# Optimization experiments

Hardware: AMD Instinct MI355X
Metric: run time of the kernel (lower is better)

Reference implementation:

```python
import jax, jax.numpy as jnp
import numpy as np

K = 5  # kernel_size

def _extract_patches(x):
    # TF extract_patches, SAME padding, stride 1, rate 1.
    # x: (B,H,W,C) -> (B,H,W,K*K,C); patch index i is row-major over (kh,kw),
    # channel d is the fastest-varying dim, matching TF's flatten order.
    p = K // 2
    xp = jnp.pad(x, ((0, 0), (p, p), (p, p), (0, 0)))
    B, H, W, C = x.shape
    pats = [xp[:, i:i + H, j:j + W, :] for i in range(K) for j in range(K)]
    return jnp.stack(pats, axis=3)

def setup_inputs() -> dict:
    key = jax.random.key(0)
    k1, k2, k3, k4 = jax.random.split(key, 4)
    B, H, W, C, F = 8, 250, 250, 4, 16
    return {
        "x": jax.random.normal(k1, (B, H, W, C), jnp.float32),
        "kernel": jax.random.normal(k2, (K, K, C, F), jnp.float32) * 0.05,
        "quad_kernel": jax.random.normal(k3, (C, K * K, K * K, F), jnp.float32) * 0.02,
        "bias": jax.random.normal(k4, (F,), jnp.float32) * 0.01,
    }

def reference(x, kernel, quad_kernel, bias):
    # Quadratic (Volterra) term: V[b,h,w,o] = sum_{i,j,d} p[bhwid] p[bhwjd] W[d,i,j,o]
    # (einsum 'abcid,abcjd,dijo->abcdo' followed by reduce_sum over d).
    patches = _extract_patches(x)  # (B,H,W,25,C)
    C = x.shape[-1]
    quad = 0.0
    for d in range(C):  # small fixed channel loop avoids a (B,H,W,25,C,F) intermediate
        pd = patches[..., d]                                   # (B,H,W,25)
        s = jnp.einsum('bhwj,ijo->bhwio', pd, quad_kernel[d])  # (B,H,W,25,F)
        quad = quad + jnp.einsum('bhwi,bhwio->bhwo', pd, s)    # (B,H,W,F)
    # Linear conv term (SAME padding, stride 1)
    lin = jax.lax.conv_general_dilated(
        x, kernel, window_strides=(1, 1), padding='SAME',
        dimension_numbers=('NHWC', 'HWIO', 'NHWC'))
    return quad + lin + bias
```

## Files before the change

### kernel.cpp

```cpp
#include <hip/hip_runtime.h>
#include <utility>


typedef _Float16 half2 __attribute__((ext_vector_type(2)));
typedef _Float16 half4 __attribute__((ext_vector_type(4)));
typedef _Float16 half8 __attribute__((ext_vector_type(8)));
typedef float floatx4 __attribute__((ext_vector_type(4)));

#define BB 8
#define HH 250
#define WW 250
#define NF 16
#define NSLOT_PAIR 181
#define NSLOT_LIN  13
#define NCHUNK     49
#define NFRAG      (NCHUNK * 64)

#define TW 64
#define TH 8
#define XW (TW + 4)
#define XH (TH + 4)
#define XSZ (XW * XH)

__host__ __device__ constexpr int slot_i(int s) {
    int i = 0, base = 0;
    while (base + (13 - (i >> 1)) <= s) { base += 13 - (i >> 1); ++i; }
    return i;
}
__host__ __device__ constexpr int slot_g(int s) {
    int i = 0, base = 0;
    while (base + (13 - (i >> 1)) <= s) { base += 13 - (i >> 1); ++i; }
    return (i >> 1) + (s - base);
}

__global__ void prep_frags(const float* __restrict__ lin_w,
                           const float* __restrict__ quad_w,
                           _Float16* __restrict__ fragB) {
    const int c = blockIdx.x;
    const int lane = threadIdx.x;
    const int n = lane & 15;
    const int d = lane >> 4;
    half8 frag;
    #pragma unroll
    for (int e = 0; e < 8; ++e) {
        const int f = c * 8 + e;
        const int s = f >> 1, hf = f & 1;
        float v = 0.f;
        if (s < NSLOT_PAIR) {
            int i = 0, base = 0;
            while (base + (13 - (i >> 1)) <= s) { base += 13 - (i >> 1); ++i; }
            const int g = (i >> 1) + (s - base);
            const int j = 2 * g + hf;
            if (j == i)
                v = quad_w[((d * 25 + i) * 25 + i) * 16 + n];
            else if (j > i && j < 25)
                v = quad_w[((d * 25 + i) * 25 + j) * 16 + n]
                  + quad_w[((d * 25 + j) * 25 + i) * 16 + n];
        } else if (s < NSLOT_PAIR + NSLOT_LIN) {
            const int j = 2 * (s - NSLOT_PAIR) + hf;
            if (j < 25) v = lin_w[(j * 4 + d) * 16 + n];
        }
        frag[e] = (_Float16)v;
    }
    *(half8*)(fragB + (c * 64 + lane) * 8) = frag;
}

__device__ __forceinline__ half2 pk(float lo, float hi) {
    return __builtin_bit_cast(half2, __builtin_amdgcn_cvt_pkrtz(lo, hi));
}

template<int S>
__device__ __forceinline__ half2 slotval(const half2 (&pd2)[13]) {
    if constexpr (S < NSLOT_PAIR) {
        constexpr int i = slot_i(S), g = slot_g(S);
        constexpr int ir = i >> 1, ih = i & 1;
        const half2 src = pd2[ir];
        const half2 bi = {src[ih], src[ih]};
        return bi * pd2[g];
    } else if constexpr (S < NSLOT_PAIR + NSLOT_LIN) {
        return pd2[S - NSLOT_PAIR];
    } else {
        return half2{(_Float16)0.f, (_Float16)0.f};
    }
}

template<int C>
__device__ __forceinline__ half8 make_frag(const half2 (&pd2)[13]) {
    const half2 a0 = slotval<C * 4 + 0>(pd2);
    const half2 a1 = slotval<C * 4 + 1>(pd2);
    const half2 a2 = slotval<C * 4 + 2>(pd2);
    const half2 a3 = slotval<C * 4 + 3>(pd2);
    const half4 lo = __builtin_shufflevector(a0, a1, 0, 1, 2, 3);
    const half4 hi = __builtin_shufflevector(a2, a3, 0, 1, 2, 3);
    return __builtin_shufflevector(lo, hi, 0, 1, 2, 3, 4, 5, 6, 7);
}

template<size_t... Cs>
__device__ __forceinline__ void gemm_all(
    const half2 (&p0)[13], const half2 (&p1)[13],
    const half2 (&p2)[13], const half2 (&p3)[13],
    const _Float16* sBlane,
    floatx4& a0, floatx4& a1, floatx4& a2, floatx4& a3,
    std::index_sequence<Cs...>) {
    (([&] {
        constexpr int C = (int)Cs;
        const half8 bf = *(const half8*)(sBlane + C * 64 * 8);
        a0 = __builtin_amdgcn_mfma_f32_16x16x32_f16(make_frag<C>(p0), bf, a0, 0, 0, 0);
        a1 = __builtin_amdgcn_mfma_f32_16x16x32_f16(make_frag<C>(p1), bf, a1, 0, 0, 0);
        a2 = __builtin_amdgcn_mfma_f32_16x16x32_f16(make_frag<C>(p2), bf, a2, 0, 0, 0);
        a3 = __builtin_amdgcn_mfma_f32_16x16x32_f16(make_frag<C>(p3), bf, a3, 0, 0, 0);
    }()), ...);
}

__device__ __forceinline__ void patch_from_lds(const float* xt, int base,
                                               half2 (&pd2)[13]) {
    float pf[26];
    pf[25] = 0.f;
    #pragma unroll
    for (int kh = 0; kh < 5; ++kh)
        #pragma unroll
        for (int kw = 0; kw < 5; ++kw)
            pf[kh * 5 + kw] = xt[base + kh * XW + kw];
    #pragma unroll
    for (int t = 0; t < 13; ++t) pd2[t] = pk(pf[2 * t], pf[2 * t + 1]);
}

__global__ __launch_bounds__(512, 4) void convquad_gemm(
    const float* __restrict__ x,
    const float* __restrict__ bias,
    const _Float16* __restrict__ fragB,
    float* __restrict__ out)
{
    __shared__ float xt[4 * XSZ];
    __shared__ __align__(16) _Float16 sB[NFRAG * 8];

    const int w0 = blockIdx.x * TW;
    const int h0 = blockIdx.y * TH;
    const int b  = blockIdx.z;

    {
        const float4* src = (const float4*)fragB;
        float4* dst = (float4*)sB;
        #pragma unroll
        for (int t = threadIdx.x; t < NFRAG * 8 / 8; t += 512) dst[t] = src[t];
    }

    #pragma unroll 2
    for (int p = threadIdx.x; p < XSZ; p += 512) {
        const int hh = p / XW, ww = p % XW;
        const int r = h0 + hh - 2, c = w0 + ww - 2;
        float4 v = make_float4(0.f, 0.f, 0.f, 0.f);
        if ((unsigned)r < (unsigned)HH && (unsigned)c < (unsigned)WW)
            v = ((const float4*)x)[(b * HH + r) * WW + c];
        xt[0 * XSZ + p] = v.x;
        xt[1 * XSZ + p] = v.y;
        xt[2 * XSZ + p] = v.z;
        xt[3 * XSZ + p] = v.w;
    }
    __syncthreads();

    const int lane = threadIdx.x & 63;
    const int wave = threadIdx.x >> 6;
    const int m = lane & 15;
    const int q = lane >> 4;

    const int base0 = q * XSZ + wave * XW + m;
    half2 pd0[13], pd1[13], pd2[13], pd3[13];
    patch_from_lds(xt, base0,      pd0);
    patch_from_lds(xt, base0 + 16, pd1);
    patch_from_lds(xt, base0 + 32, pd2);
    patch_from_lds(xt, base0 + 48, pd3);

    const float bo = bias[m];
    floatx4 acc0 = {bo, bo, bo, bo};
    floatx4 acc1 = acc0, acc2 = acc0, acc3 = acc0;

    gemm_all(pd0, pd1, pd2, pd3, sB + lane * 8,
             acc0, acc1, acc2, acc3, std::make_index_sequence<NCHUNK>{});

    const int h = h0 + wave;
    if (h < HH) {
        const int rowbase = (b * HH + h) * WW;
        #pragma unroll
        for (int r = 0; r < 4; ++r) {
            const int wA = w0 + q * 4 + r;
            if (wA < WW) out[(rowbase + wA) * NF + m] = acc0[r];
            const int wB = w0 + 16 + q * 4 + r;
            if (wB < WW) out[(rowbase + wB) * NF + m] = acc1[r];
            const int wC = w0 + 32 + q * 4 + r;
            if (wC < WW) out[(rowbase + wC) * NF + m] = acc2[r];
            const int wD = w0 + 48 + q * 4 + r;
            if (wD < WW) out[(rowbase + wD) * NF + m] = acc3[r];
        }
    }
}

extern "C" void kernel_launch(void* const* d_in, const int* in_sizes, int n_in,
                              void* d_out, int out_size, void* d_ws, size_t ws_size,
                              hipStream_t stream) {
    const float* x      = (const float*)d_in[0];
    const float* lin_w  = (const float*)d_in[1];
    const float* quad_w = (const float*)d_in[2];
    const float* bias   = (const float*)d_in[3];
    float* out = (float*)d_out;
    _Float16* fragB = (_Float16*)d_ws;

    prep_frags<<<dim3(NCHUNK), dim3(64), 0, stream>>>(lin_w, quad_w, fragB);

    dim3 grid((WW + TW - 1) / TW, (HH + TH - 1) / TH, BB);
    convquad_gemm<<<grid, dim3(512), 0, stream>>>(x, bias, fragB, out);
}
```

Baseline: 104.0 us.

## Make GEMM kernel persistent with register-prefetched next tile input

Replaces the one-block-per-tile grid with 512 persistent blocks that each process two tiles. The weight fragments are loaded into LDS only once per block, and the next tile's input halo is prefetched into registers while the current tile's MFMA work runs. The goal is to cut the repeated sB fill and hide global load latency, at the cost of extra barriers and higher register pressure.

```diff
diff --git a/kernel.cpp b/kernel.cpp
--- a/kernel.cpp
+++ b/kernel.cpp
@@ -21,6 +21,12 @@
 #define XW (TW + 4)
 #define XH (TH + 4)
 #define XSZ (XW * XH)
+
+#define NBLK     512
+#define NTILE_W  4
+#define NTILE_H  32
+#define NTILES   (BB * NTILE_H * NTILE_W)
+#define NT       (NTILES / NBLK)
 
 __host__ __device__ constexpr int slot_i(int s) {
     int i = 0, base = 0;
@@ -125,6 +131,49 @@
     for (int t = 0; t < 13; ++t) pd2[t] = pk(pf[2 * t], pf[2 * t + 1]);
 }
 
+__device__ __forceinline__ void tile_coords(int T, int& b, int& h0, int& w0) {
+    b = T >> 7;
+    const int rem = T & 127;
+    h0 = (rem >> 2) * TH;
+    w0 = (rem & 3) * TW;
+}
+
+__device__ __forceinline__ void xload_regs(const float* __restrict__ x,
+                                           int b, int h0, int w0,
+                                           float4& v0, float4& v1) {
+    const int p0 = threadIdx.x;
+    {
+        const int hh = p0 / XW, ww = p0 % XW;
+        const int r = h0 + hh - 2, c = w0 + ww - 2;
+        v0 = make_float4(0.f, 0.f, 0.f, 0.f);
+        if ((unsigned)r < (unsigned)HH && (unsigned)c < (unsigned)WW)
+            v0 = ((const float4*)x)[(b * HH + r) * WW + c];
+    }
+    const int p1 = p0 + 512;
+    v1 = make_float4(0.f, 0.f, 0.f, 0.f);
+    if (p1 < XSZ) {
+        const int hh = p1 / XW, ww = p1 % XW;
+        const int r = h0 + hh - 2, c = w0 + ww - 2;
+        if ((unsigned)r < (unsigned)HH && (unsigned)c < (unsigned)WW)
+            v1 = ((const float4*)x)[(b * HH + r) * WW + c];
+    }
+}
+
+__device__ __forceinline__ void xwrite_lds(float* xt, const float4& v0, const float4& v1) {
+    const int p0 = threadIdx.x;
+    xt[0 * XSZ + p0] = v0.x;
+    xt[1 * XSZ + p0] = v0.y;
+    xt[2 * XSZ + p0] = v0.z;
+    xt[3 * XSZ + p0] = v0.w;
+    const int p1 = p0 + 512;
+    if (p1 < XSZ) {
+        xt[0 * XSZ + p1] = v1.x;
+        xt[1 * XSZ + p1] = v1.y;
+        xt[2 * XSZ + p1] = v1.z;
+        xt[3 * XSZ + p1] = v1.w;
+    }
+}
+
 __global__ __launch_bounds__(512, 4) void convquad_gemm(
     const float* __restrict__ x,
     const float* __restrict__ bias,
@@ -134,9 +183,16 @@
     __shared__ float xt[4 * XSZ];
     __shared__ __align__(16) _Float16 sB[NFRAG * 8];
 
-    const int w0 = blockIdx.x * TW;
-    const int h0 = blockIdx.y * TH;
-    const int b  = blockIdx.z;
+    const int lane = threadIdx.x & 63;
+    const int wave = threadIdx.x >> 6;
+    const int m = lane & 15;
+    const int q = lane >> 4;
+    const float bo = bias[m];
+
+    int b, h0, w0;
+    tile_coords(blockIdx.x, b, h0, w0);
+    float4 v0, v1;
+    xload_regs(x, b, h0, w0, v0, v1);
 
     {
         const float4* src = (const float4*)fragB;
@@ -144,53 +200,50 @@
         #pragma unroll
         for (int t = threadIdx.x; t < NFRAG * 8 / 8; t += 512) dst[t] = src[t];
     }
-
-    #pragma unroll 2
-    for (int p = threadIdx.x; p < XSZ; p += 512) {
-        const int hh = p / XW, ww = p % XW;
-        const int r = h0 + hh - 2, c = w0 + ww - 2;
-        float4 v = make_float4(0.f, 0.f, 0.f, 0.f);
-        if ((unsigned)r < (unsigned)HH && (unsigned)c < (unsigned)WW)
-            v = ((const float4*)x)[(b * HH + r) * WW + c];
-        xt[0 * XSZ + p] = v.x;
-        xt[1 * XSZ + p] = v.y;
-        xt[2 * XSZ + p] = v.z;
-        xt[3 * XSZ + p] = v.w;
-    }
+    xwrite_lds(xt, v0, v1);
     __syncthreads();
 
-    const int lane = threadIdx.x & 63;
-    const int wave = threadIdx.x >> 6;
-    const int m = lane & 15;
-    const int q = lane >> 4;
-
-    const int base0 = q * XSZ + wave * XW + m;
-    half2 pd0[13], pd1[13], pd2[13], pd3[13];
-    patch_from_lds(xt, base0,      pd0);
-    patch_from_lds(xt, base0 + 16, pd1);
-    patch_from_lds(xt, base0 + 32, pd2);
-    patch_from_lds(xt, base0 + 48, pd3);
-
-    const float bo = bias[m];
-    floatx4 acc0 = {bo, bo, bo, bo};
-    floatx4 acc1 = acc0, acc2 = acc0, acc3 = acc0;
-
-    gemm_all(pd0, pd1, pd2, pd3, sB + lane * 8,
-             acc0, acc1, acc2, acc3, std::make_index_sequence<NCHUNK>{});
-
-    const int h = h0 + wave;
-    if (h < HH) {
-        const int rowbase = (b * HH + h) * WW;
-        #pragma unroll
-        for (int r = 0; r < 4; ++r) {
-            const int wA = w0 + q * 4 + r;
-            if (wA < WW) out[(rowbase + wA) * NF + m] = acc0[r];
-            const int wB = w0 + 16 + q * 4 + r;
-            if (wB < WW) out[(rowbase + wB) * NF + m] = acc1[r];
-            const int wC = w0 + 32 + q * 4 + r;
-            if (wC < WW) out[(rowbase + wC) * NF + m] = acc2[r];
-            const int wD = w0 + 48 + q * 4 + r;
-            if (wD < WW) out[(rowbase + wD) * NF + m] = acc3[r];
+    #pragma unroll 1
+    for (int t = 0; t < NT; ++t) {
+        int bn, h0n, w0n;
+        if (t + 1 < NT) {
+            tile_coords(blockIdx.x + (t + 1) * NBLK, bn, h0n, w0n);
+            xload_regs(x, bn, h0n, w0n, v0, v1);
+        }
+
+        const int base0 = q * XSZ + wave * XW + m;
+        half2 pd0[13], pd1[13], pd2[13], pd3[13];
+        patch_from_lds(xt, base0,      pd0);
+        patch_from_lds(xt, base0 + 16, pd1);
+        patch_from_lds(xt, base0 + 32, pd2);
+        patch_from_lds(xt, base0 + 48, pd3);
+
+        floatx4 acc0 = {bo, bo, bo, bo};
+        floatx4 acc1 = acc0, acc2 = acc0, acc3 = acc0;
+        gemm_all(pd0, pd1, pd2, pd3, sB + lane * 8,
+                 acc0, acc1, acc2, acc3, std::make_index_sequence<NCHUNK>{});
+
+        const int h = h0 + wave;
+        if (h < HH) {
+            const int rowbase = (b * HH + h) * WW;
+            #pragma unroll
+            for (int r = 0; r < 4; ++r) {
+                const int wA = w0 + q * 4 + r;
+                if (wA < WW) out[(rowbase + wA) * NF + m] = acc0[r];
+                const int wB = w0 + 16 + q * 4 + r;
+                if (wB < WW) out[(rowbase + wB) * NF + m] = acc1[r];
+                const int wC = w0 + 32 + q * 4 + r;
+                if (wC < WW) out[(rowbase + wC) * NF + m] = acc2[r];
+                const int wD = w0 + 48 + q * 4 + r;
+                if (wD < WW) out[(rowbase + wD) * NF + m] = acc3[r];
+            }
+        }
+
+        if (t + 1 < NT) {
+            b = bn; h0 = h0n; w0 = w0n;
+            __syncthreads();
+            xwrite_lds(xt, v0, v1);
+            __syncthreads();
         }
     }
 }
@@ -207,6 +260,5 @@
 
     prep_frags<<<dim3(NCHUNK), dim3(64), 0, stream>>>(lin_w, quad_w, fragB);
 
-    dim3 grid((WW + TW - 1) / TW, (HH + TH - 1) / TH, BB);
-    convquad_gemm<<<grid, dim3(512), 0, stream>>>(x, bias, fragB, out);
-}
+    convquad_gemm<<<dim3(NBLK), dim3(512), 0, stream>>>(x, bias, fragB, out);
+}
```

Result: no change. 102.4 us (-1.5%).
